# Performance work log

Measured on AMD Instinct MI355X. Metric: run time of the kernel, lower is better.

## Reference

```python
import jax, jax.numpy as jnp
import numpy as np
import math

N_HEAD = 16
N_EMBD = 1024
HEAD_DIM = N_EMBD // N_HEAD  # 64
B, T = 4, 2048


def setup_inputs() -> dict:
    key = jax.random.key(0)
    k1, k2, k3, k4, k5 = jax.random.split(key, 5)
    x = jax.random.normal(k1, (B, T, N_EMBD), dtype=jnp.float32)
    # RoPE frequency tables, shape (T, head_dim//2)
    freqs_cos = jax.random.uniform(k2, (T, HEAD_DIM // 2), dtype=jnp.float32)
    freqs_sin = jax.random.uniform(k3, (T, HEAD_DIM // 2), dtype=jnp.float32)
    # Learned params (nn.Linear stores weight as (out, in); y = x @ W.T)
    w_attn = jax.random.normal(k4, (3 * N_EMBD, N_EMBD), dtype=jnp.float32) * (1.0 / math.sqrt(N_EMBD))
    w_proj = jax.random.normal(k5, (N_EMBD, N_EMBD), dtype=jnp.float32) * (1.0 / math.sqrt(N_EMBD))
    return {"x": x, "freqs_cos": freqs_cos, "freqs_sin": freqs_sin,
            "w_attn": w_attn, "w_proj": w_proj}


def _rope(t, cos, sin):
    # t: (B, T, H, D); interleaved complex split, matching reshape(...,-1,2).unbind(-1)
    b, s, h, d = t.shape
    tr = t.reshape(b, s, h, d // 2, 2)
    t_r, t_i = tr[..., 0], tr[..., 1]
    cos = cos[None, :, None, :]  # (1, T, 1, D/2)
    sin = sin[None, :, None, :]
    o_r = t_r * cos - t_i * sin
    o_i = t_r * sin + t_i * cos
    return jnp.stack([o_r, o_i], axis=-1).reshape(b, s, h, d)


def reference(x, freqs_cos, freqs_sin, w_attn, w_proj):
    b, t, c = x.shape
    qkv = x @ w_attn.T                      # (B, T, 3C)
    q, k, v = jnp.split(qkv, 3, axis=-1)
    q = q.reshape(b, t, N_HEAD, HEAD_DIM)
    k = k.reshape(b, t, N_HEAD, HEAD_DIM)
    v = v.reshape(b, t, N_HEAD, HEAD_DIM)
    q = _rope(q, freqs_cos, freqs_sin)
    k = _rope(k, freqs_cos, freqs_sin)
    # (B, H, T, D)
    q = q.transpose(0, 2, 1, 3)
    k = k.transpose(0, 2, 1, 3)
    v = v.transpose(0, 2, 1, 3)
    scale = 1.0 / math.sqrt(HEAD_DIM)
    att = jnp.einsum('bhqd,bhkd->bhqk', q, k) * scale
    causal = jnp.tril(jnp.ones((t, t), dtype=bool))
    att = jnp.where(causal[None, None], att, jnp.finfo(att.dtype).min)
    att = jax.nn.softmax(att, axis=-1)
    # dropout layers are identity in eval mode
    y = jnp.einsum('bhqk,bhkd->bhqd', att, v)
    y = y.transpose(0, 2, 1, 3).reshape(b, t, c)
    return y @ w_proj.T
```

## Files before the change

kernel.cpp:

```cpp
#include <hip/hip_runtime.h>
#include <hip/hip_bf16.h>


typedef __attribute__((ext_vector_type(8))) short short8;
typedef __attribute__((ext_vector_type(4))) float floatx4;
typedef __attribute__((ext_vector_type(4))) unsigned short ushort4v;

#define AS3(p) ((__attribute__((address_space(3))) char*)(p))
#define AS1(p) ((const __attribute__((address_space(1))) char*)(p))

__device__ __forceinline__ float bf2f(unsigned int u) {
    union { unsigned int i; float f; } v; v.i = u << 16; return v.f;
}
__device__ __forceinline__ unsigned short f2bf(float f) {
    union { float f; unsigned int i; } v; v.f = f;
    const unsigned int x = v.i;
    return (unsigned short)((x + 0x7fffu + ((x >> 16) & 1u)) >> 16);
}

__global__ void f32_to_bf16_kernel(const float* __restrict__ in,
                                   unsigned short* __restrict__ out, int n4) {
    const int i = blockIdx.x * blockDim.x + threadIdx.x;
    if (i >= n4) return;
    const float4 v = ((const float4*)in)[i];
    ushort4v o;
    o.x = f2bf(v.x); o.y = f2bf(v.y); o.z = f2bf(v.z); o.w = f2bf(v.w);
    ((ushort4v*)out)[i] = o;
}

template<int OUT_F32, int A_BHTD>
__global__ __launch_bounds__(256) void gemm_bt_kernel(
    const unsigned short* __restrict__ A, const unsigned short* __restrict__ B,
    void* __restrict__ C, int M, int N, int Kd) {
    __shared__ __align__(16) unsigned short alds[2][4096];
    __shared__ __align__(16) unsigned short blds[2][4096];
    const int tid = threadIdx.x;
    const int w = tid >> 6, lane = tid & 63;
    const int lg = lane >> 4, li = lane & 15;
    const int wm = w >> 1, wn = w & 1;
    const int bm = blockIdx.y, bn = blockIdx.x;
    const int nk = Kd >> 5;
    const size_t abase = (size_t)bm * 128 * Kd;
    const size_t bbase = (size_t)bn * 128 * Kd;

    auto stage = [&](int buf, int kt) {
        const int k0 = kt * 32;
#pragma unroll
        for (int i = 0; i < 2; ++i) {
            const int e = w * 1024 + i * 512 + lane * 8;
            const int row = e >> 5, col = e & 31;
            const unsigned short* asrc;
            if constexpr (A_BHTD) {
                const int R = bm * 128 + row;
                asrc = A + ((size_t)((R >> 11) * 16 + (k0 >> 6)) * 2048 + (R & 2047)) * 64 +
                       (k0 & 63) + col;
            } else {
                asrc = A + abase + (size_t)row * Kd + k0 + col;
            }
            __builtin_amdgcn_global_load_lds(AS1(asrc),
                                             AS3(&alds[buf][w * 1024 + i * 512]), 16, 0, 0);
            __builtin_amdgcn_global_load_lds(AS1(B + bbase + (size_t)row * Kd + k0 + col),
                                             AS3(&blds[buf][w * 1024 + i * 512]), 16, 0, 0);
        }
    };

    floatx4 acc[4][4];
#pragma unroll
    for (int a = 0; a < 4; ++a)
#pragma unroll
        for (int b2 = 0; b2 < 4; ++b2) acc[a][b2] = (floatx4){0.f, 0.f, 0.f, 0.f};

    stage(0, 0);
    __syncthreads();
    for (int kt = 0; kt < nk; ++kt) {
        const int cur = kt & 1;
        if (kt + 1 < nk) stage(cur ^ 1, kt + 1);
        short8 af[4], bfr[4];
#pragma unroll
        for (int f = 0; f < 4; ++f) {
            af[f]  = *(const short8*)&alds[cur][(wm * 64 + f * 16 + li) * 32 + lg * 8];
            bfr[f] = *(const short8*)&blds[cur][(wn * 64 + f * 16 + li) * 32 + lg * 8];
        }
#pragma unroll
        for (int fm = 0; fm < 4; ++fm)
#pragma unroll
            for (int fn = 0; fn < 4; ++fn)
                acc[fm][fn] = __builtin_amdgcn_mfma_f32_16x16x32_bf16(
                    af[fm], bfr[fn], acc[fm][fn], 0, 0, 0);
        __syncthreads();
    }

    const int r0 = bm * 128 + wm * 64, c0 = bn * 128 + wn * 64;
#pragma unroll
    for (int fm = 0; fm < 4; ++fm)
#pragma unroll
        for (int fn = 0; fn < 4; ++fn)
#pragma unroll
            for (int i = 0; i < 4; ++i) {
                const int row = r0 + fm * 16 + lg * 4 + i;
                const int col = c0 + fn * 16 + li;
                const float v = acc[fm][fn][i];
                if (OUT_F32) ((float*)C)[(size_t)row * N + col] = v;
                else ((unsigned short*)C)[(size_t)row * N + col] = f2bf(v);
            }
}

__global__ void rope_split_kernel(const unsigned short* __restrict__ qkv,
                                  const float* __restrict__ fc, const float* __restrict__ fs,
                                  unsigned short* __restrict__ qr, unsigned short* __restrict__ kr) {
    const int idx = blockIdx.x * 256 + threadIdx.x;
    const int dp = idx & 31;
    const int h = (idx >> 5) & 15;
    const int t = (idx >> 9) & 2047;
    const int b = idx >> 20;
    const size_t row = (size_t)(b * 2048 + t) * 3072;
    const unsigned int q2 = *(const unsigned int*)&qkv[row + h * 64 + 2 * dp];
    const unsigned int k2 = *(const unsigned int*)&qkv[row + 1024 + h * 64 + 2 * dp];
    const float c = fc[t * 32 + dp], s = fs[t * 32 + dp];
    const float qre = bf2f(q2 & 0xffffu), qim = bf2f(q2 >> 16);
    const float kre = bf2f(k2 & 0xffffu), kim = bf2f(k2 >> 16);
    const unsigned int qo = (unsigned int)f2bf(qre * c - qim * s) |
                            ((unsigned int)f2bf(qre * s + qim * c) << 16);
    const unsigned int ko = (unsigned int)f2bf(kre * c - kim * s) |
                            ((unsigned int)f2bf(kre * s + kim * c) << 16);
    const size_t dst = ((size_t)(b * 16 + h) * 2048 + t) * 64 + 2 * dp;
    *(unsigned int*)&qr[dst] = qo;
    *(unsigned int*)&kr[dst] = ko;
}

__global__ void v_trans_kernel(const unsigned short* __restrict__ qkv,
                               unsigned short* __restrict__ vt) {
    __shared__ __align__(16) unsigned short tile[64 * 72];
    const int tt = blockIdx.x, bh = blockIdx.y;
    const int b = bh >> 4, h = bh & 15;
    const int tid = threadIdx.x;
    const int trow = tid >> 2, dcol = (tid & 3) * 16;
    const unsigned short* src =
        &qkv[((size_t)(b * 2048 + tt * 64 + trow)) * 3072 + 2048 + h * 64 + dcol];
    *(short8*)&tile[trow * 72 + dcol] = *(const short8*)src;
    *(short8*)&tile[trow * 72 + dcol + 8] = *(const short8*)(src + 8);
    __syncthreads();
    const int drow = tid >> 2, tcol = (tid & 3) * 16;
    short8 o0, o1;
#pragma unroll
    for (int j = 0; j < 8; ++j) o0[j] = (short)tile[(tcol + j) * 72 + drow];
#pragma unroll
    for (int j = 0; j < 8; ++j) o1[j] = (short)tile[(tcol + 8 + j) * 72 + drow];
    unsigned short* dst = &vt[((size_t)(bh * 64 + drow)) * 2048 + tt * 64 + tcol];
    *(short8*)dst = o0;
    *(short8*)(dst + 8) = o1;
}

__global__ __launch_bounds__(256) void attn_kernel(
    const unsigned short* __restrict__ Q, const unsigned short* __restrict__ K,
    const unsigned short* __restrict__ Vt, unsigned short* __restrict__ O) {
    __shared__ __align__(16) unsigned short kls[64 * 72];
    __shared__ __align__(16) unsigned short vtls[64 * 72];
    __shared__ __align__(16) unsigned short pls[4][16 * 72];
    const int id = blockIdx.x;
    const int xcd = id & 7, jj = (id >> 3) & 7, ip = id >> 6;
    const int bh = xcd * 8 + jj;
    const int qtA = ip, qtB = 31 - ip;
    const unsigned short* Qp = Q + (size_t)bh * 2048 * 64;
    const unsigned short* Kp = K + (size_t)bh * 2048 * 64;
    const unsigned short* Vp = Vt + (size_t)bh * 64 * 2048;
    unsigned short* Op = O + (size_t)bh * 2048 * 64;
    const int tid = threadIdx.x, w = tid >> 6, lane = tid & 63;
    const int lg = lane >> 4, li = lane & 15;

    short8 qfA[2], qfB[2];
    {
        const int rA = qtA * 64 + w * 16 + li, rB = qtB * 64 + w * 16 + li;
#pragma unroll
        for (int kc = 0; kc < 2; ++kc) {
            qfA[kc] = *(const short8*)&Qp[(size_t)rA * 64 + kc * 32 + lg * 8];
            qfB[kc] = *(const short8*)&Qp[(size_t)rB * 64 + kc * 32 + lg * 8];
        }
    }

    floatx4 oA[4], oB[4];
#pragma unroll
    for (int dt = 0; dt < 4; ++dt) {
        oA[dt] = (floatx4){0.f, 0.f, 0.f, 0.f};
        oB[dt] = (floatx4){0.f, 0.f, 0.f, 0.f};
    }
    float mA[4] = {-1e30f, -1e30f, -1e30f, -1e30f}, lA[4] = {0.f, 0.f, 0.f, 0.f};
    float mB[4] = {-1e30f, -1e30f, -1e30f, -1e30f}, lB[4] = {0.f, 0.f, 0.f, 0.f};

    const int srow = tid >> 2, scol = (tid & 3) * 16;
    short8 ks0, ks1, vs0, vs1;
    auto loadT = [&](int kv) {
        const unsigned short* kp = &Kp[((size_t)(kv * 64 + srow)) * 64 + scol];
        ks0 = *(const short8*)kp;
        ks1 = *(const short8*)(kp + 8);
        const unsigned short* vp = &Vp[(size_t)srow * 2048 + kv * 64 + scol];
        vs0 = *(const short8*)vp;
        vs1 = *(const short8*)(vp + 8);
    };
    auto storeT = [&]() {
        *(short8*)&kls[srow * 72 + scol] = ks0;
        *(short8*)&kls[srow * 72 + scol + 8] = ks1;
        *(short8*)&vtls[srow * 72 + scol] = vs0;
        *(short8*)&vtls[srow * 72 + scol + 8] = vs1;
    };

    auto process = [&](const short8 (&qf)[2], floatx4 (&oacc)[4], float (&mrun)[4],
                       float (&lrun)[4], bool diag) {
        floatx4 s[4];
        __builtin_amdgcn_s_setprio(1);
#pragma unroll
        for (int k4 = 0; k4 < 4; ++k4) {
            floatx4 a = (floatx4){0.f, 0.f, 0.f, 0.f};
#pragma unroll
            for (int kc = 0; kc < 2; ++kc) {
                const short8 kf = *(const short8*)&kls[(k4 * 16 + li) * 72 + kc * 32 + lg * 8];
                a = __builtin_amdgcn_mfma_f32_16x16x32_bf16(qf[kc], kf, a, 0, 0, 0);
            }
            s[k4] = a;
        }
        __builtin_amdgcn_s_setprio(0);
#pragma unroll
        for (int k4 = 0; k4 < 4; ++k4)
#pragma unroll
            for (int i = 0; i < 4; ++i) {
                float sv = s[k4][i] * 0.125f;
                if (diag && (k4 * 16 + li > w * 16 + lg * 4 + i)) sv = -1e30f;
                s[k4][i] = sv;
            }

        float mnew[4];
#pragma unroll
        for (int i = 0; i < 4; ++i) {
            float m0 = fmaxf(fmaxf(s[0][i], s[1][i]), fmaxf(s[2][i], s[3][i]));
#pragma unroll
            for (int msk = 1; msk <= 8; msk <<= 1) m0 = fmaxf(m0, __shfl_xor(m0, msk));
            mnew[i] = fmaxf(m0, mrun[i]);
        }
#pragma unroll
        for (int i = 0; i < 4; ++i) {
            const float al = __expf(mrun[i] - mnew[i]);
            mrun[i] = mnew[i];
            lrun[i] *= al;
#pragma unroll
            for (int dt = 0; dt < 4; ++dt) oacc[dt][i] *= al;
        }
#pragma unroll
        for (int i = 0; i < 4; ++i) {
            float r = 0.f;
#pragma unroll
            for (int k4 = 0; k4 < 4; ++k4) {
                const float p = __expf(s[k4][i] - mnew[i]);
                s[k4][i] = p;
                r += p;
            }
#pragma unroll
            for (int msk = 1; msk <= 8; msk <<= 1) r += __shfl_xor(r, msk);
            lrun[i] += r;
        }

#pragma unroll
        for (int k4 = 0; k4 < 4; ++k4)
#pragma unroll
            for (int i = 0; i < 4; ++i)
                pls[w][(lg * 4 + i) * 72 + k4 * 16 + li] = f2bf(s[k4][i]);
        asm volatile("s_waitcnt lgkmcnt(0)" ::: "memory");

        short8 pf[2];
#pragma unroll
        for (int kc = 0; kc < 2; ++kc)
            pf[kc] = *(const short8*)&pls[w][li * 72 + kc * 32 + lg * 8];
        __builtin_amdgcn_s_setprio(1);
#pragma unroll
        for (int dt = 0; dt < 4; ++dt)
#pragma unroll
            for (int kc = 0; kc < 2; ++kc) {
                const short8 vf = *(const short8*)&vtls[(dt * 16 + li) * 72 + kc * 32 + lg * 8];
                oacc[dt] = __builtin_amdgcn_mfma_f32_16x16x32_bf16(pf[kc], vf, oacc[dt], 0, 0, 0);
            }
        __builtin_amdgcn_s_setprio(0);
    };

    loadT(0);
    storeT();
    __syncthreads();
    for (int kv = 0; kv <= qtB; ++kv) {
        if (kv < qtB) loadT(kv + 1);
        if (kv <= qtA) process(qfA, oA, mA, lA, kv == qtA);
        process(qfB, oB, mB, lB, kv == qtB);
        if (kv < qtB) {
            __syncthreads();
            storeT();
            __syncthreads();
        }
    }

#pragma unroll
    for (int dt = 0; dt < 4; ++dt)
#pragma unroll
        for (int i = 0; i < 4; ++i) {
            const int qgA = qtA * 64 + w * 16 + lg * 4 + i;
            Op[(size_t)qgA * 64 + dt * 16 + li] = f2bf(oA[dt][i] / lA[i]);
            const int qgB = qtB * 64 + w * 16 + lg * 4 + i;
            Op[(size_t)qgB * 64 + dt * 16 + li] = f2bf(oB[dt][i] / lB[i]);
        }
}

extern "C" void kernel_launch(void* const* d_in, const int* in_sizes, int n_in,
                              void* d_out, int out_size, void* d_ws, size_t ws_size,
                              hipStream_t stream) {
    const float* x  = (const float*)d_in[0];
    const float* fc = (const float*)d_in[1];
    const float* fs = (const float*)d_in[2];
    const float* wa = (const float*)d_in[3];
    const float* wp = (const float*)d_in[4];
    char* ws = (char*)d_ws;
    unsigned short* xb   = (unsigned short*)(ws);
    unsigned short* wab  = (unsigned short*)(ws + 16777216);
    unsigned short* wpb  = (unsigned short*)(ws + 23068672);
    unsigned short* qkvb = (unsigned short*)(ws + 25165824);
    unsigned short* qr   = (unsigned short*)(ws + 75497472);
    unsigned short* kr   = (unsigned short*)(ws + 92274688);
    unsigned short* vt   = (unsigned short*)(ws + 109051904);
    unsigned short* ob   = xb;

    f32_to_bf16_kernel<<<8192, 256, 0, stream>>>(x, xb, 2097152);
    f32_to_bf16_kernel<<<3072, 256, 0, stream>>>(wa, wab, 786432);
    f32_to_bf16_kernel<<<1024, 256, 0, stream>>>(wp, wpb, 262144);
    gemm_bt_kernel<0, 0><<<dim3(24, 64), 256, 0, stream>>>(xb, wab, qkvb, 8192, 3072, 1024);
    rope_split_kernel<<<16384, 256, 0, stream>>>(qkvb, fc, fs, qr, kr);
    v_trans_kernel<<<dim3(32, 64), 256, 0, stream>>>(qkvb, vt);
    attn_kernel<<<1024, 256, 0, stream>>>(qr, kr, vt, ob);
    gemm_bt_kernel<1, 1><<<dim3(8, 64), 256, 0, stream>>>(ob, wpb, d_out, 8192, 1024, 1024);
}
```

Baseline: 345.8 us.

## Fuse softmax row-sum into PV MFMA, share K fragments across two query tiles

Several changes to the attention kernel. The 1/sqrt(d) scale is folded into Q during RoPE, removing a per-score multiply. A ones-row is appended to the V tile so an extra MFMA column produces the softmax denominator, replacing the shuffle-based row-sum reductions. K fragments are loaded once and reused for both query tiles, with the two tiles' softmax and PV interleaved. P is packed with v_cvt_pk_bf16_f32. The cost is one more MFMA column per tile, more registers, and double-buffered P in LDS, which may lower occupancy.

Measured after the change: 370.6 us. +7.2%, slower.

```diff
diff --git a/kernel.cpp b/kernel.cpp
--- a/kernel.cpp
+++ b/kernel.cpp
@@ -1,5 +1,6 @@
 #include <hip/hip_runtime.h>
 #include <hip/hip_bf16.h>
+#include <type_traits>
 
 
 typedef __attribute__((ext_vector_type(8))) short short8;
@@ -8,6 +9,8 @@
 
 #define AS3(p) ((__attribute__((address_space(3))) char*)(p))
 #define AS1(p) ((const __attribute__((address_space(1))) char*)(p))
+
+template <int N> using IC = std::integral_constant<int, N>;
 
 __device__ __forceinline__ float bf2f(unsigned int u) {
     union { unsigned int i; float f; } v; v.i = u << 16; return v.f;
@@ -16,6 +19,11 @@
     union { float f; unsigned int i; } v; v.f = f;
     const unsigned int x = v.i;
     return (unsigned short)((x + 0x7fffu + ((x >> 16) & 1u)) >> 16);
+}
+__device__ __forceinline__ unsigned int cvtpk_bf16(float lo, float hi) {
+    unsigned int r;
+    asm volatile("v_cvt_pk_bf16_f32 %0, %1, %2" : "=v"(r) : "v"(lo), "v"(hi));
+    return r;
 }
 
 __global__ void f32_to_bf16_kernel(const float* __restrict__ in,
@@ -119,8 +127,8 @@
     const float c = fc[t * 32 + dp], s = fs[t * 32 + dp];
     const float qre = bf2f(q2 & 0xffffu), qim = bf2f(q2 >> 16);
     const float kre = bf2f(k2 & 0xffffu), kim = bf2f(k2 >> 16);
-    const unsigned int qo = (unsigned int)f2bf(qre * c - qim * s) |
-                            ((unsigned int)f2bf(qre * s + qim * c) << 16);
+    const unsigned int qo = (unsigned int)f2bf((qre * c - qim * s) * 0.125f) |
+                            ((unsigned int)f2bf((qre * s + qim * c) * 0.125f) << 16);
     const unsigned int ko = (unsigned int)f2bf(kre * c - kim * s) |
                             ((unsigned int)f2bf(kre * s + kim * c) << 16);
     const size_t dst = ((size_t)(b * 16 + h) * 2048 + t) * 64 + 2 * dp;
@@ -155,8 +163,8 @@
     const unsigned short* __restrict__ Q, const unsigned short* __restrict__ K,
     const unsigned short* __restrict__ Vt, unsigned short* __restrict__ O) {
     __shared__ __align__(16) unsigned short kls[64 * 72];
-    __shared__ __align__(16) unsigned short vtls[64 * 72];
-    __shared__ __align__(16) unsigned short pls[4][16 * 72];
+    __shared__ __align__(16) unsigned short vtls[80 * 72];
+    __shared__ __align__(16) unsigned short pls[4][2][16 * 72];
     const int id = blockIdx.x;
     const int xcd = id & 7, jj = (id >> 3) & 7, ip = id >> 6;
     const int bh = xcd * 8 + jj;
@@ -168,24 +176,26 @@
     const int tid = threadIdx.x, w = tid >> 6, lane = tid & 63;
     const int lg = lane >> 4, li = lane & 15;
 
-    short8 qfA[2], qfB[2];
+    short8 qf2[2][2];
     {
         const int rA = qtA * 64 + w * 16 + li, rB = qtB * 64 + w * 16 + li;
 #pragma unroll
         for (int kc = 0; kc < 2; ++kc) {
-            qfA[kc] = *(const short8*)&Qp[(size_t)rA * 64 + kc * 32 + lg * 8];
-            qfB[kc] = *(const short8*)&Qp[(size_t)rB * 64 + kc * 32 + lg * 8];
-        }
-    }
-
-    floatx4 oA[4], oB[4];
-#pragma unroll
-    for (int dt = 0; dt < 4; ++dt) {
-        oA[dt] = (floatx4){0.f, 0.f, 0.f, 0.f};
-        oB[dt] = (floatx4){0.f, 0.f, 0.f, 0.f};
-    }
-    float mA[4] = {-1e30f, -1e30f, -1e30f, -1e30f}, lA[4] = {0.f, 0.f, 0.f, 0.f};
-    float mB[4] = {-1e30f, -1e30f, -1e30f, -1e30f}, lB[4] = {0.f, 0.f, 0.f, 0.f};
+            qf2[0][kc] = *(const short8*)&Qp[(size_t)rA * 64 + kc * 32 + lg * 8];
+            qf2[1][kc] = *(const short8*)&Qp[(size_t)rB * 64 + kc * 32 + lg * 8];
+        }
+    }
+
+    floatx4 oacc2[2][5];
+    float m2[2][4];
+#pragma unroll
+    for (int st = 0; st < 2; ++st) {
+#pragma unroll
+        for (int dt = 0; dt < 5; ++dt) oacc2[st][dt] = (floatx4){0.f, 0.f, 0.f, 0.f};
+#pragma unroll
+        for (int i = 0; i < 4; ++i) m2[st][i] = -1e30f;
+    }
+    unsigned short* pb[2] = {&pls[w][0][0], &pls[w][1][0]};
 
     const int srow = tid >> 2, scol = (tid & 3) * 16;
     short8 ks0, ks1, vs0, vs1;
@@ -204,89 +214,109 @@
         *(short8*)&vtls[srow * 72 + scol + 8] = vs1;
     };
 
-    auto process = [&](const short8 (&qf)[2], floatx4 (&oacc)[4], float (&mrun)[4],
-                       float (&lrun)[4], bool diag) {
-        floatx4 s[4];
+    auto proc = [&](auto S0C, auto S1C, bool dA, bool dB) {
+        constexpr int S0 = decltype(S0C)::value;
+        constexpr int S1 = decltype(S1C)::value;
+        const bool dg[2] = {dA, dB};
+        short8 kfr[4][2];
+#pragma unroll
+        for (int k4 = 0; k4 < 4; ++k4)
+#pragma unroll
+            for (int kc = 0; kc < 2; ++kc)
+                kfr[k4][kc] = *(const short8*)&kls[(k4 * 16 + li) * 72 + kc * 32 + lg * 8];
+        floatx4 s2[2][4];
         __builtin_amdgcn_s_setprio(1);
 #pragma unroll
-        for (int k4 = 0; k4 < 4; ++k4) {
-            floatx4 a = (floatx4){0.f, 0.f, 0.f, 0.f};
-#pragma unroll
-            for (int kc = 0; kc < 2; ++kc) {
-                const short8 kf = *(const short8*)&kls[(k4 * 16 + li) * 72 + kc * 32 + lg * 8];
-                a = __builtin_amdgcn_mfma_f32_16x16x32_bf16(qf[kc], kf, a, 0, 0, 0);
-            }
-            s[k4] = a;
-        }
+        for (int st = S0; st < S1; ++st)
+#pragma unroll
+            for (int k4 = 0; k4 < 4; ++k4) {
+                floatx4 a = (floatx4){0.f, 0.f, 0.f, 0.f};
+#pragma unroll
+                for (int kc = 0; kc < 2; ++kc)
+                    a = __builtin_amdgcn_mfma_f32_16x16x32_bf16(qf2[st][kc], kfr[k4][kc], a,
+                                                                0, 0, 0);
+                s2[st][k4] = a;
+            }
         __builtin_amdgcn_s_setprio(0);
 #pragma unroll
-        for (int k4 = 0; k4 < 4; ++k4)
+        for (int st = S0; st < S1; ++st)
+            if (dg[st]) {
+#pragma unroll
+                for (int k4 = 0; k4 < 4; ++k4)
+#pragma unroll
+                    for (int i = 0; i < 4; ++i)
+                        if (k4 * 16 + li > w * 16 + lg * 4 + i) s2[st][k4][i] = -1e30f;
+            }
+        float mnew[2][4];
+#pragma unroll
+        for (int st = S0; st < S1; ++st)
 #pragma unroll
             for (int i = 0; i < 4; ++i) {
-                float sv = s[k4][i] * 0.125f;
-                if (diag && (k4 * 16 + li > w * 16 + lg * 4 + i)) sv = -1e30f;
-                s[k4][i] = sv;
-            }
-
-        float mnew[4];
-#pragma unroll
-        for (int i = 0; i < 4; ++i) {
-            float m0 = fmaxf(fmaxf(s[0][i], s[1][i]), fmaxf(s[2][i], s[3][i]));
-#pragma unroll
-            for (int msk = 1; msk <= 8; msk <<= 1) m0 = fmaxf(m0, __shfl_xor(m0, msk));
-            mnew[i] = fmaxf(m0, mrun[i]);
-        }
-#pragma unroll
-        for (int i = 0; i < 4; ++i) {
-            const float al = __expf(mrun[i] - mnew[i]);
-            mrun[i] = mnew[i];
-            lrun[i] *= al;
-#pragma unroll
-            for (int dt = 0; dt < 4; ++dt) oacc[dt][i] *= al;
-        }
-#pragma unroll
-        for (int i = 0; i < 4; ++i) {
-            float r = 0.f;
-#pragma unroll
-            for (int k4 = 0; k4 < 4; ++k4) {
-                const float p = __expf(s[k4][i] - mnew[i]);
-                s[k4][i] = p;
-                r += p;
-            }
-#pragma unroll
-            for (int msk = 1; msk <= 8; msk <<= 1) r += __shfl_xor(r, msk);
-            lrun[i] += r;
-        }
-
-#pragma unroll
-        for (int k4 = 0; k4 < 4; ++k4)
-#pragma unroll
-            for (int i = 0; i < 4; ++i)
-                pls[w][(lg * 4 + i) * 72 + k4 * 16 + li] = f2bf(s[k4][i]);
+                float m0 = fmaxf(fmaxf(s2[st][0][i], s2[st][1][i]),
+                                 fmaxf(s2[st][2][i], s2[st][3][i]));
+#pragma unroll
+                for (int msk = 1; msk <= 8; msk <<= 1) m0 = fmaxf(m0, __shfl_xor(m0, msk));
+                mnew[st][i] = fmaxf(m0, m2[st][i]);
+            }
+#pragma unroll
+        for (int st = S0; st < S1; ++st)
+#pragma unroll
+            for (int i = 0; i < 4; ++i) {
+                const float al = __expf(m2[st][i] - mnew[st][i]);
+                m2[st][i] = mnew[st][i];
+#pragma unroll
+                for (int dt = 0; dt < 5; ++dt) oacc2[st][dt][i] *= al;
+            }
+#pragma unroll
+        for (int st = S0; st < S1; ++st)
+#pragma unroll
+            for (int k4 = 0; k4 < 4; ++k4)
+#pragma unroll
+                for (int i = 0; i < 4; ++i)
+                    s2[st][k4][i] = __expf(s2[st][k4][i] - mnew[st][i]);
+#pragma unroll
+        for (int st = S0; st < S1; ++st)
+#pragma unroll
+            for (int k4 = 0; k4 < 4; ++k4)
+#pragma unroll
+                for (int i2 = 0; i2 < 4; i2 += 2) {
+                    const unsigned int u = cvtpk_bf16(s2[st][k4][i2], s2[st][k4][i2 + 1]);
+                    pb[st][(lg * 4 + i2) * 72 + k4 * 16 + li] = (unsigned short)u;
+                    pb[st][(lg * 4 + i2 + 1) * 72 + k4 * 16 + li] =
+                        (unsigned short)(u >> 16);
+                }
         asm volatile("s_waitcnt lgkmcnt(0)" ::: "memory");
-
-        short8 pf[2];
-#pragma unroll
-        for (int kc = 0; kc < 2; ++kc)
-            pf[kc] = *(const short8*)&pls[w][li * 72 + kc * 32 + lg * 8];
+        short8 pf2[2][2];
+#pragma unroll
+        for (int st = S0; st < S1; ++st)
+#pragma unroll
+            for (int kc = 0; kc < 2; ++kc)
+                pf2[st][kc] = *(const short8*)&pb[st][li * 72 + kc * 32 + lg * 8];
         __builtin_amdgcn_s_setprio(1);
 #pragma unroll
-        for (int dt = 0; dt < 4; ++dt)
+        for (int dt = 0; dt < 5; ++dt)
 #pragma unroll
             for (int kc = 0; kc < 2; ++kc) {
                 const short8 vf = *(const short8*)&vtls[(dt * 16 + li) * 72 + kc * 32 + lg * 8];
-                oacc[dt] = __builtin_amdgcn_mfma_f32_16x16x32_bf16(pf[kc], vf, oacc[dt], 0, 0, 0);
+#pragma unroll
+                for (int st = S0; st < S1; ++st)
+                    oacc2[st][dt] = __builtin_amdgcn_mfma_f32_16x16x32_bf16(
+                        pf2[st][kc], vf, oacc2[st][dt], 0, 0, 0);
             }
         __builtin_amdgcn_s_setprio(0);
     };
 
+    for (int ix = tid; ix < 16 * 72; ix += 256) {
+        const int r = ix / 72, c = ix - r * 72;
+        vtls[(64 + r) * 72 + c] = (r == 0) ? (unsigned short)0x3f80 : (unsigned short)0;
+    }
     loadT(0);
     storeT();
     __syncthreads();
     for (int kv = 0; kv <= qtB; ++kv) {
         if (kv < qtB) loadT(kv + 1);
-        if (kv <= qtA) process(qfA, oA, mA, lA, kv == qtA);
-        process(qfB, oB, mB, lB, kv == qtB);
+        if (kv <= qtA) proc(IC<0>{}, IC<2>{}, kv == qtA, false);
+        else           proc(IC<1>{}, IC<2>{}, false, kv == qtB);
         if (kv < qtB) {
             __syncthreads();
             storeT();
@@ -295,14 +325,22 @@
     }
 
 #pragma unroll
-    for (int dt = 0; dt < 4; ++dt)
+    for (int st = 0; st < 2; ++st) {
+        const int qt = st ? qtB : qtA;
+        float rs[4];
 #pragma unroll
         for (int i = 0; i < 4; ++i) {
-            const int qgA = qtA * 64 + w * 16 + lg * 4 + i;
-            Op[(size_t)qgA * 64 + dt * 16 + li] = f2bf(oA[dt][i] / lA[i]);
-            const int qgB = qtB * 64 + w * 16 + lg * 4 + i;
-            Op[(size_t)qgB * 64 + dt * 16 + li] = f2bf(oB[dt][i] / lB[i]);
-        }
+            const float l = __shfl(oacc2[st][4][i], lane & 48);
+            rs[i] = 1.f / l;
+        }
+#pragma unroll
+        for (int dt = 0; dt < 4; ++dt)
+#pragma unroll
+            for (int i = 0; i < 4; ++i) {
+                const int qg = qt * 64 + w * 16 + lg * 4 + i;
+                Op[(size_t)qg * 64 + dt * 16 + li] = f2bf(oacc2[st][dt][i] * rs[i]);
+            }
+    }
 }
 
 extern "C" void kernel_launch(void* const* d_in, const int* in_sizes, int n_in,
```
